# Kernel tuning notes

Hardware: AMD Instinct MI355X
Metric: run time of the kernel (lower is better)

The kernel has to match this reference:

```python
import jax, jax.numpy as jnp
import numpy as np

B, D, L = 512, 512, 24

def setup_inputs() -> dict:
    key = jax.random.key(0)
    k1, k2 = jax.random.split(key)
    source = jax.random.normal(k1, (B, D), dtype=jnp.float32)
    s_labels = jax.random.randint(k2, (B, L), 0, 2, dtype=jnp.int32)
    return {"source": source, "s_labels": s_labels}

def reference(source, s_labels):
    margin = 0.0
    squared = False
    # pairwise squared euclidean distances, (B, B)
    diff = source[:, None, :] - source[None, :, :]          # (B, B, D)
    dist = jnp.clip(jnp.sum(diff * diff, axis=-1), 0.0)     # (B, B)
    if not squared:
        zmask = (dist == 0.0).astype(dist.dtype)
        dist = jnp.sqrt(dist + zmask * 1e-16) * (1.0 - zmask)
    # triplet validity mask: labels[i]==labels[j] (share a label) and labels[i]!=labels[k]
    lab = s_labels.astype(jnp.float32)
    sim = (lab @ lab.T > 0).astype(jnp.float32)              # (B, B)
    mask = sim[:, :, None] * (1.0 - sim[:, None, :])         # (B, B, B)
    # euclidean branch: d_ap - (1 - margin) * d_an
    triplet = dist[:, :, None] - (1.0 - margin) * dist[:, None, :]
    triplet = jnp.clip(mask * triplet, 0.0)                  # (B, B, B)
    num_positive = jnp.sum((triplet > 1e-16).astype(jnp.float32))
    return jnp.sum(triplet) / (num_positive + 1e-16)
```

## Files before the change

### kernel.cpp

```cpp
#include <hip/hip_runtime.h>

#define BN 512
#define DD 512
#define LL 24
#define NB 512
#define NT 512


__global__ __launch_bounds__(NT) void row_kernel(
    const float* __restrict__ S, const int* __restrict__ labels,
    float* __restrict__ slots)
{
    __shared__ unsigned mask_lds[BN];
    __shared__ float    d_lds[BN];
    __shared__ int      anyneg_s;

    const int t    = threadIdx.x;
    const int lane = t & 63;
    const int w    = t >> 6;
    const int i    = blockIdx.x;

    if (t == 0) anyneg_s = 0;

    {
        const int4* lab4 = (const int4*)(labels + (size_t)t * LL);
        unsigned m = 0;
#pragma unroll
        for (int v = 0; v < 6; v++) {
            int4 x = lab4[v];
            m |= (x.x ? 1u : 0u) << (4 * v)
               | (x.y ? 1u : 0u) << (4 * v + 1)
               | (x.z ? 1u : 0u) << (4 * v + 2)
               | (x.w ? 1u : 0u) << (4 * v + 3);
        }
        mask_lds[t] = m;
    }
    __syncthreads();

    const unsigned mi = mask_lds[i];
    if ((mi & mask_lds[t]) == 0u) anyneg_s = 1;
    __syncthreads();

    float sum = 0.f; unsigned cnt = 0u;

    if (anyneg_s) {
        const float* si_p = S + (size_t)i * DD + 8 * lane;
        const float4 si0 = *(const float4*)si_p;
        const float4 si1 = *(const float4*)(si_p + 4);

        const int jbase = w << 6;
        for (int jj = 0; jj < 32; jj++) {
            const int jA = jbase + jj, jB = jA + 32;
            const float* pa = S + (size_t)jA * DD + 8 * lane;
            const float* pb = S + (size_t)jB * DD + 8 * lane;
            const float4 a0 = *(const float4*)pa, a1 = *(const float4*)(pa + 4);
            const float4 b0 = *(const float4*)pb, b1 = *(const float4*)(pb + 4);

            float dA, dB;
            {
                float v;
                v = a0.x - si0.x; dA  = v * v;   v = b0.x - si0.x; dB  = v * v;
                v = a0.y - si0.y; dA += v * v;   v = b0.y - si0.y; dB += v * v;
                v = a0.z - si0.z; dA += v * v;   v = b0.z - si0.z; dB += v * v;
                v = a0.w - si0.w; dA += v * v;   v = b0.w - si0.w; dB += v * v;
                v = a1.x - si1.x; dA += v * v;   v = b1.x - si1.x; dB += v * v;
                v = a1.y - si1.y; dA += v * v;   v = b1.y - si1.y; dB += v * v;
                v = a1.z - si1.z; dA += v * v;   v = b1.z - si1.z; dB += v * v;
                v = a1.w - si1.w; dA += v * v;   v = b1.w - si1.w; dB += v * v;
            }
#pragma unroll
            for (int off = 1; off < 64; off <<= 1) {
                dA += __shfl_xor(dA, off);
                dB += __shfl_xor(dB, off);
            }
            if (lane == 0) {
                d_lds[jA] = sqrtf(fmaxf(dA, 0.f));
                d_lds[jB] = sqrtf(fmaxf(dB, 0.f));
            }
        }
        __syncthreads();

        if (w == 0) {
            unsigned long long pb[8]; float dv[8];
#pragma unroll
            for (int c = 0; c < 8; c++) {
                pb[c] = __ballot((mi & mask_lds[c * 64 + lane]) != 0u);
                dv[c] = d_lds[c * 64 + lane];
            }
#pragma unroll
            for (int c = 0; c < 8; c++) {
                unsigned long long nb = ~pb[c];
                while (nb) {
                    const int k = __ffsll(nb) - 1;
                    nb &= nb - 1;
                    const float dk = __shfl(dv[c], k);
#pragma unroll
                    for (int c2 = 0; c2 < 8; c2++) {
                        if ((pb[c2] >> lane) & 1ull) {
                            const float v = dv[c2] - dk;
                            sum += fmaxf(v, 0.0f);
                            cnt += (v > 1e-16f) ? 1u : 0u;
                        }
                    }
                }
            }
#pragma unroll
            for (int off = 32; off > 0; off >>= 1) {
                sum += __shfl_down(sum, off);
                cnt += __shfl_down(cnt, off);
            }
        }
    }

    if (t == 0) {
        slots[2 * i]                  = sum;
        ((unsigned*)slots)[2 * i + 1] = cnt;
    }
}

__global__ __launch_bounds__(256) void finalize_kernel(
    const float* __restrict__ slots, float* __restrict__ out)
{
    __shared__ float    wsum[4];
    __shared__ unsigned wcnt[4];
    const int t    = threadIdx.x;
    const int lane = t & 63;
    const int w    = t >> 6;

    float s = 0.f; unsigned c = 0u;
    for (int b = t; b < NB; b += 256) {
        s += slots[2 * b];
        c += ((const unsigned*)slots)[2 * b + 1];
    }
#pragma unroll
    for (int off = 32; off > 0; off >>= 1) {
        s += __shfl_down(s, off);
        c += __shfl_down(c, off);
    }
    if (lane == 0) { wsum[w] = s; wcnt[w] = c; }
    __syncthreads();
    if (t == 0) {
        s = wsum[0] + wsum[1] + wsum[2] + wsum[3];
        c = wcnt[0] + wcnt[1] + wcnt[2] + wcnt[3];
        out[0] = s / ((float)c + 1e-16f);
    }
}

extern "C" void kernel_launch(void* const* d_in, const int* in_sizes, int n_in,
                              void* d_out, int out_size, void* d_ws, size_t ws_size,
                              hipStream_t stream) {
    const float* src    = (const float*)d_in[0];
    const int*   labels = (const int*)d_in[1];
    float* slots = (float*)d_ws;

    hipLaunchKernelGGL(row_kernel,      dim3(NB), dim3(NT),  0, stream, src, labels, slots);
    hipLaunchKernelGGL(finalize_kernel, dim3(1),  dim3(256), 0, stream, slots, (float*)d_out);
}
```

Measured before the change: 82.81 us.

## Compute row distances with bf16 MFMA via norm expansion

Replaces the per-pair fp32 difference-squared reduction with the expansion ||a||^2 + ||b||^2 - 2ab. The dot products run on bf16 16x16x32 MFMA instructions, with one 16-row j-tile per wave and a register prefetch of the next k-slice. The block size drops from 512 to 256 threads, and rows with no negatives now exit early. The intent is to remove the long chain of cross-lane shuffle reductions. The cost is bf16 rounding in the dot product, which can shift distances and change which triplets count as positive.

```diff
diff --git a/kernel.cpp b/kernel.cpp
--- a/kernel.cpp
+++ b/kernel.cpp
@@ -1,11 +1,35 @@
 #include <hip/hip_runtime.h>
+#include <hip/hip_bf16.h>
 
 #define BN 512
 #define DD 512
 #define LL 24
 #define NB 512
-#define NT 512
-
+#define NT 256
+
+typedef __attribute__((ext_vector_type(8))) short short8;
+typedef __attribute__((ext_vector_type(4))) float f32x4;
+
+
+__device__ __forceinline__ unsigned pk_bf16(float lo, float hi) {
+    __hip_bfloat162 p = __float22bfloat162_rn(make_float2(lo, hi));
+    unsigned u;
+    __builtin_memcpy(&u, &p, 4);
+    return u;
+}
+
+__device__ __forceinline__ short8 pack8_pk(float4 x, float4 y, float& nrm) {
+    nrm = fmaf(x.x, x.x, nrm); nrm = fmaf(x.y, x.y, nrm);
+    nrm = fmaf(x.z, x.z, nrm); nrm = fmaf(x.w, x.w, nrm);
+    nrm = fmaf(y.x, y.x, nrm); nrm = fmaf(y.y, y.y, nrm);
+    nrm = fmaf(y.z, y.z, nrm); nrm = fmaf(y.w, y.w, nrm);
+    union { uint4 u; short8 s; } cv;
+    cv.u.x = pk_bf16(x.x, x.y);
+    cv.u.y = pk_bf16(x.z, x.w);
+    cv.u.z = pk_bf16(y.x, y.y);
+    cv.u.w = pk_bf16(y.z, y.w);
+    return cv.s;
+}
 
 __global__ __launch_bounds__(NT) void row_kernel(
     const float* __restrict__ S, const int* __restrict__ labels,
@@ -13,6 +37,7 @@
 {
     __shared__ unsigned mask_lds[BN];
     __shared__ float    d_lds[BN];
+    __shared__ uint4    si_bf4[64];
     __shared__ int      anyneg_s;
 
     const int t    = threadIdx.x;
@@ -22,8 +47,10 @@
 
     if (t == 0) anyneg_s = 0;
 
-    {
-        const int4* lab4 = (const int4*)(labels + (size_t)t * LL);
+#pragma unroll
+    for (int rr = 0; rr < 2; rr++) {
+        const int row = t + rr * NT;
+        const int4* lab4 = (const int4*)(labels + (size_t)row * LL);
         unsigned m = 0;
 #pragma unroll
         for (int v = 0; v < 6; v++) {
@@ -33,82 +60,98 @@
                | (x.z ? 1u : 0u) << (4 * v + 2)
                | (x.w ? 1u : 0u) << (4 * v + 3);
         }
-        mask_lds[t] = m;
+        mask_lds[row] = m;
+    }
+
+    const float* sip = S + (size_t)i * DD + 8 * lane;
+    const float4 s0 = *(const float4*)sip;
+    const float4 s1 = *(const float4*)(sip + 4);
+    float ni = 0.f;
+    ni = fmaf(s0.x, s0.x, ni); ni = fmaf(s0.y, s0.y, ni);
+    ni = fmaf(s0.z, s0.z, ni); ni = fmaf(s0.w, s0.w, ni);
+    ni = fmaf(s1.x, s1.x, ni); ni = fmaf(s1.y, s1.y, ni);
+    ni = fmaf(s1.z, s1.z, ni); ni = fmaf(s1.w, s1.w, ni);
+#pragma unroll
+    for (int off = 1; off < 64; off <<= 1) ni += __shfl_xor(ni, off);
+    if (w == 0) {
+        uint4 pk;
+        pk.x = pk_bf16(s0.x, s0.y); pk.y = pk_bf16(s0.z, s0.w);
+        pk.z = pk_bf16(s1.x, s1.y); pk.w = pk_bf16(s1.z, s1.w);
+        si_bf4[lane] = pk;
     }
     __syncthreads();
 
     const unsigned mi = mask_lds[i];
-    if ((mi & mask_lds[t]) == 0u) anyneg_s = 1;
+    if (((mi & mask_lds[t]) == 0u) || ((mi & mask_lds[t + NT]) == 0u)) anyneg_s = 1;
+    __syncthreads();
+
+    if (!anyneg_s) {
+        if (t == 0) { slots[2 * i] = 0.f; ((unsigned*)slots)[2 * i + 1] = 0u; }
+        return;
+    }
+
+    const int r = lane & 15;
+    const int q = lane >> 4;
+#pragma unroll
+    for (int tt = 0; tt < 8; tt++) {
+        const int jb = (w + 4 * tt) * 16;
+        const float* pB = S + (size_t)(jb + r) * DD + q * 8;
+
+        f32x4 acc = {0.f, 0.f, 0.f, 0.f};
+        float nB = 0.f;
+        float4 bx = *(const float4*)pB, by = *(const float4*)(pB + 4);
+
+        for (int k0 = 0; k0 < DD; k0 += 32) {
+            float4 nbx, nby;
+            const int kn = k0 + 32;
+            if (kn < DD) {
+                nbx = *(const float4*)(pB + kn);
+                nby = *(const float4*)(pB + kn + 4);
+            }
+            union { uint4 u; short8 s; } av;
+            av.u = si_bf4[(k0 >> 3) + q];
+            short8 bf = pack8_pk(bx, by, nB);
+            acc = __builtin_amdgcn_mfma_f32_16x16x32_bf16(av.s, bf, acc, 0, 0, 0);
+            bx = nbx; by = nby;
+        }
+        nB += __shfl_xor(nB, 16); nB += __shfl_xor(nB, 32);
+        if (q == 0) {
+            const int j = jb + r;
+            const float d2 = ni + nB - 2.f * acc[0];
+            d_lds[j] = (j == i) ? 0.f : sqrtf(fmaxf(d2, 0.f));
+        }
+    }
     __syncthreads();
 
     float sum = 0.f; unsigned cnt = 0u;
-
-    if (anyneg_s) {
-        const float* si_p = S + (size_t)i * DD + 8 * lane;
-        const float4 si0 = *(const float4*)si_p;
-        const float4 si1 = *(const float4*)(si_p + 4);
-
-        const int jbase = w << 6;
-        for (int jj = 0; jj < 32; jj++) {
-            const int jA = jbase + jj, jB = jA + 32;
-            const float* pa = S + (size_t)jA * DD + 8 * lane;
-            const float* pb = S + (size_t)jB * DD + 8 * lane;
-            const float4 a0 = *(const float4*)pa, a1 = *(const float4*)(pa + 4);
-            const float4 b0 = *(const float4*)pb, b1 = *(const float4*)(pb + 4);
-
-            float dA, dB;
-            {
-                float v;
-                v = a0.x - si0.x; dA  = v * v;   v = b0.x - si0.x; dB  = v * v;
-                v = a0.y - si0.y; dA += v * v;   v = b0.y - si0.y; dB += v * v;
-                v = a0.z - si0.z; dA += v * v;   v = b0.z - si0.z; dB += v * v;
-                v = a0.w - si0.w; dA += v * v;   v = b0.w - si0.w; dB += v * v;
-                v = a1.x - si1.x; dA += v * v;   v = b1.x - si1.x; dB += v * v;
-                v = a1.y - si1.y; dA += v * v;   v = b1.y - si1.y; dB += v * v;
-                v = a1.z - si1.z; dA += v * v;   v = b1.z - si1.z; dB += v * v;
-                v = a1.w - si1.w; dA += v * v;   v = b1.w - si1.w; dB += v * v;
-            }
-#pragma unroll
-            for (int off = 1; off < 64; off <<= 1) {
-                dA += __shfl_xor(dA, off);
-                dB += __shfl_xor(dB, off);
-            }
-            if (lane == 0) {
-                d_lds[jA] = sqrtf(fmaxf(dA, 0.f));
-                d_lds[jB] = sqrtf(fmaxf(dB, 0.f));
-            }
-        }
-        __syncthreads();
-
-        if (w == 0) {
-            unsigned long long pb[8]; float dv[8];
-#pragma unroll
-            for (int c = 0; c < 8; c++) {
-                pb[c] = __ballot((mi & mask_lds[c * 64 + lane]) != 0u);
-                dv[c] = d_lds[c * 64 + lane];
-            }
-#pragma unroll
-            for (int c = 0; c < 8; c++) {
-                unsigned long long nb = ~pb[c];
-                while (nb) {
-                    const int k = __ffsll(nb) - 1;
-                    nb &= nb - 1;
-                    const float dk = __shfl(dv[c], k);
-#pragma unroll
-                    for (int c2 = 0; c2 < 8; c2++) {
-                        if ((pb[c2] >> lane) & 1ull) {
-                            const float v = dv[c2] - dk;
-                            sum += fmaxf(v, 0.0f);
-                            cnt += (v > 1e-16f) ? 1u : 0u;
-                        }
+    if (w == 0) {
+        unsigned long long pb[8]; float dv[8];
+#pragma unroll
+        for (int c = 0; c < 8; c++) {
+            pb[c] = __ballot((mi & mask_lds[c * 64 + lane]) != 0u);
+            dv[c] = d_lds[c * 64 + lane];
+        }
+#pragma unroll
+        for (int c = 0; c < 8; c++) {
+            unsigned long long nb = ~pb[c];
+            while (nb) {
+                const int k = __ffsll(nb) - 1;
+                nb &= nb - 1;
+                const float dk = __shfl(dv[c], k);
+#pragma unroll
+                for (int c2 = 0; c2 < 8; c2++) {
+                    if ((pb[c2] >> lane) & 1ull) {
+                        const float v = dv[c2] - dk;
+                        sum += fmaxf(v, 0.0f);
+                        cnt += (v > 1e-16f) ? 1u : 0u;
                     }
                 }
             }
-#pragma unroll
-            for (int off = 32; off > 0; off >>= 1) {
-                sum += __shfl_down(sum, off);
-                cnt += __shfl_down(cnt, off);
-            }
+        }
+#pragma unroll
+        for (int off = 32; off > 0; off >>= 1) {
+            sum += __shfl_down(sum, off);
+            cnt += __shfl_down(cnt, off);
         }
     }
 
```

After: 114.0 us. 37.6% more time.
